# Optimization experiments

Measured on AMD Instinct MI355X. Metric: run time of the kernel, lower is better.

The kernel has to match this reference:

```python
import jax, jax.numpy as jnp
import numpy as np

HEADS = 8
DIM = 512
SCALE = (DIM // HEADS) ** (-0.5)  # 0.125


def setup_inputs() -> dict:
    key = jax.random.key(0)
    k1, k2, k3, k4 = jax.random.split(key, 4)
    B, C, H, W = 4, DIM, 96, 96
    x = jax.random.normal(k1, (B, C, H, W), dtype=jnp.float32)
    # 1x1 conv weights collapsed to matrices [out_ch, in_ch]
    w_qkv = jax.random.normal(k2, (3 * DIM, DIM), dtype=jnp.float32) * (DIM ** -0.5)
    w_out = jax.random.normal(k3, (DIM, DIM), dtype=jnp.float32) * (DIM ** -0.5)
    b_out = jax.random.normal(k4, (DIM,), dtype=jnp.float32) * 0.01
    return {"x": x, "w_qkv": w_qkv, "w_out": w_out, "b_out": b_out}


def reference(x, w_qkv, w_out, b_out):
    # axis='height' branch of the original forward
    b, c, h, w = x.shape
    heads = HEADS
    d = c // heads
    # 1x1 conv == per-pixel GEMM: [B,3C,H,W]
    qkv = jnp.einsum('bchw,oc->bohw', x, w_qkv)
    # 'b (qkv heads d) x y -> qkv b heads x y d'
    qkv = qkv.reshape(b, 3, heads, d, h, w)
    qkv = jnp.transpose(qkv, (1, 0, 2, 4, 5, 3))  # [3, b, heads, h, w, d]
    q, k, v = qkv[0], qkv[1], qkv[2]
    # attention along the width axis, batched over (b, heads, row x)
    dots = jnp.einsum('bhxid,bhxjd->bhxij', q, k) * SCALE
    attn = jax.nn.softmax(dots, axis=-1)
    out = jnp.einsum('bhxij,bhxjd->bhxid', attn, v)  # [b, heads, h, w, d]
    # 'b heads x y d -> b (heads d) x y'
    out = jnp.transpose(out, (0, 1, 4, 2, 3)).reshape(b, heads * d, h, w)
    # to_out 1x1 conv with bias
    out = jnp.einsum('bchw,oc->bohw', out, w_out) + b_out[None, :, None, None]
    return out
```

## Files before the change

kernel.cpp:

```cpp
#include <hip/hip_runtime.h>

typedef unsigned short u16;
typedef unsigned int u32;
typedef __attribute__((ext_vector_type(8))) short short8;
typedef __attribute__((ext_vector_type(4))) float floatx4;

#define HEADS 8
#define DIM 512
#define HH 96
#define WW 96
#define NPIX 9216
#define M_TOT 36864
#define N_QKV 1536
#define SCALE 0.125f

__device__ __forceinline__ float b2f(u16 v){
    union{float f;u32 u;}x; x.u=((u32)v)<<16; return x.f;
}
__device__ __forceinline__ u16 f2b(float f){
    union{float f;u32 u;}x; x.f=f;
    u32 u=x.u + 0x7fffu + ((x.u>>16)&1u);
    return (u16)(u>>16);
}
__device__ __forceinline__ u32 pack2(float a,float b){
    u32 r; asm("v_cvt_pk_bf16_f32 %0, %1, %2" : "=v"(r) : "v"(a), "v"(b));
    return r;
}

__device__ __forceinline__ void gload16(const u16* g, u16* l){
    __builtin_amdgcn_global_load_lds(
        (const __attribute__((address_space(1))) u32*)g,
        (__attribute__((address_space(3))) u32*)l, 16, 0, 0);
}

__global__ void detect_dtype(const u16* __restrict__ wq, int* __restrict__ flag){
    __shared__ int cnt;
    if (threadIdx.x==0) cnt=0;
    __syncthreads();
    u16 u = wq[2*threadIdx.x];
    int e = (u>>7)&0xff;
    if (e>=100 && e<=128) atomicAdd(&cnt,1);
    __syncthreads();
    if (threadIdx.x==0) *flag = (cnt>128)?1:0;
}

__global__ __launch_bounds__(256)
void convert_w(const void* __restrict__ wq, const void* __restrict__ wo,
               const int* __restrict__ flag, u16* __restrict__ wqb, u16* __restrict__ wob){
    const int isb = *flag;
    int i = blockIdx.x*256 + threadIdx.x;
    const int nq = N_QKV*DIM;
    if (i < nq){
        wqb[i] = isb ? ((const u16*)wq)[i] : f2b(((const float*)wq)[i]);
    } else {
        int j = i - nq;
        wob[j] = isb ? ((const u16*)wo)[j] : f2b(((const float*)wo)[j]);
    }
}

__global__ __launch_bounds__(256)
void convert_x(const void* __restrict__ xv, const int* __restrict__ flag,
               u16* __restrict__ xb){
    __shared__ u16 tile[64][65];
    const int isb = *flag;
    const int p0 = blockIdx.x*64, c0 = blockIdx.y*64, b = blockIdx.z;
    const int t = threadIdx.x;
    const int pl = t&63, c4 = t>>6;
    const float* x32 = (const float*)xv;
    const u16*   x16 = (const u16*)xv;
    size_t src = ((size_t)b*DIM + c0 + c4)*NPIX + p0 + pl;
    #pragma unroll
    for (int i=0;i<16;i++){
        int cl = c4 + i*4;
        size_t s = src + (size_t)i*4*NPIX;
        tile[cl][pl] = isb ? x16[s] : f2b(x32[s]);
    }
    __syncthreads();
    const int cu = t&31, r8 = t>>5;
    u32* xb32 = (u32*)xb;
    #pragma unroll
    for (int i=0;i<8;i++){
        int pr = r8 + i*8;
        u32 v = (u32)tile[2*cu][pr] | ((u32)tile[2*cu+1][pr]<<16);
        xb32[((size_t)b*NPIX + p0 + pr)*(DIM/2) + (c0>>1) + cu] = v;
    }
}

__global__ __launch_bounds__(512, 2)
void gemm_qkv(const u16* __restrict__ A, const u16* __restrict__ B,
              u16* __restrict__ Cqk, u16* __restrict__ vt){
    __shared__ __align__(16) union ShMem {
        u16 tiles[65536];
        float ctQ[8][16][68];
        float ctV[8][16][132];
    } sh;
    u16* lds = sh.tiles;
    const int id = blockIdx.x;
    const int xcd = id & 7, slot = id >> 3;
    const int q6 = slot/6;
    const int by = xcd*18 + q6;
    const int bx = slot - q6*6;
    const int t = threadIdx.x;
    const int w = t>>6, l = t&63, lr = l&15, lq = l>>4;
    const int wm2 = w>>2, wn4 = w&3;
    const int m0 = by*256, n0 = bx*256;
    const u16* gA0 = A + (size_t)(m0 +       w*16 + lr)*DIM + lq*8;
    const u16* gA1 = A + (size_t)(m0 + 128 + w*16 + lr)*DIM + lq*8;
    const u16* gB0 = B + (size_t)(n0 +       w*16 + lr)*DIM + lq*8;
    const u16* gB1 = B + (size_t)(n0 + 128 + w*16 + lr)*DIM + lq*8;

#define STG(gp, opb, h, ko, bb) do { \
        const u16* _g = (gp) + (ko); \
        u16* _l = lds + (bb)*32768 + (opb) + ((h)*8 + w)*1024; \
        gload16(_g,      _l); \
        gload16(_g + 32, _l + 512); \
    } while(0)

    floatx4 acc[8][4] = {};
    STG(gA0, 0,     0, 0, 0);
    STG(gA1, 0,     1, 0, 0);
    STG(gB0, 16384, 0, 0, 0);
    STG(gB1, 16384, 1, 0, 0);

    #pragma unroll 1
    for (int ktile=0; ktile<8; ++ktile){
        const int cur = ktile&1, nxt = cur^1;
        const int ko = (ktile+1)*64;
        if (ktile < 7){
            STG(gA0, 0, 0, ko, nxt);
            asm volatile("s_waitcnt vmcnt(2)" ::: "memory");
        } else {
            asm volatile("s_waitcnt vmcnt(0)" ::: "memory");
        }
        __builtin_amdgcn_s_barrier();
        asm volatile("" ::: "memory");
        const u16* bA = lds + cur*32768 +         wm2*8192 + l*8;
        const u16* bB = lds + cur*32768 + 16384 + wn4*4096 + l*8;
        short8 af[4][2], blo[2][2], bhi[2][2];
        #pragma unroll
        for (int mi=0;mi<4;mi++){
            af[mi][0] = *(const short8*)(bA + mi*1024);
            af[mi][1] = *(const short8*)(bA + mi*1024 + 512);
        }
        #pragma unroll
        for (int ni=0;ni<2;ni++){
            blo[ni][0] = *(const short8*)(bB + ni*1024);
            blo[ni][1] = *(const short8*)(bB + ni*1024 + 512);
        }
        if (ktile < 7) STG(gA1, 0, 1, ko, nxt);
        asm volatile("" ::: "memory");
        __builtin_amdgcn_s_barrier();
        __builtin_amdgcn_sched_barrier(0);
        __builtin_amdgcn_s_setprio(1);
        #pragma unroll
        for (int mi=0;mi<4;mi++)
            #pragma unroll
            for (int ni=0;ni<2;ni++){
                acc[mi][ni] = __builtin_amdgcn_mfma_f32_16x16x32_bf16(af[mi][0], blo[ni][0], acc[mi][ni], 0,0,0);
                acc[mi][ni] = __builtin_amdgcn_mfma_f32_16x16x32_bf16(af[mi][1], blo[ni][1], acc[mi][ni], 0,0,0);
            }
        __builtin_amdgcn_s_setprio(0);
        __builtin_amdgcn_sched_barrier(0);
        __builtin_amdgcn_s_barrier();
        #pragma unroll
        for (int ni=0;ni<2;ni++){
            bhi[ni][0] = *(const short8*)(bB + (2+ni)*1024);
            bhi[ni][1] = *(const short8*)(bB + (2+ni)*1024 + 512);
        }
        if (ktile < 7) STG(gB0, 16384, 0, ko, nxt);
        asm volatile("" ::: "memory");
        __builtin_amdgcn_s_barrier();
        __builtin_amdgcn_sched_barrier(0);
        __builtin_amdgcn_s_setprio(1);
        #pragma unroll
        for (int mi=0;mi<4;mi++)
            #pragma unroll
            for (int ni=0;ni<2;ni++){
                acc[mi][2+ni] = __builtin_amdgcn_mfma_f32_16x16x32_bf16(af[mi][0], bhi[ni][0], acc[mi][2+ni], 0,0,0);
                acc[mi][2+ni] = __builtin_amdgcn_mfma_f32_16x16x32_bf16(af[mi][1], bhi[ni][1], acc[mi][2+ni], 0,0,0);
            }
        __builtin_amdgcn_s_setprio(0);
        __builtin_amdgcn_sched_barrier(0);
        __builtin_amdgcn_s_barrier();
        #pragma unroll
        for (int mi=0;mi<4;mi++){
            af[mi][0] = *(const short8*)(bA + (4+mi)*1024);
            af[mi][1] = *(const short8*)(bA + (4+mi)*1024 + 512);
        }
        if (ktile < 7) STG(gB1, 16384, 1, ko, nxt);
        asm volatile("" ::: "memory");
        __builtin_amdgcn_s_barrier();
        __builtin_amdgcn_sched_barrier(0);
        __builtin_amdgcn_s_setprio(1);
        #pragma unroll
        for (int mi=0;mi<4;mi++)
            #pragma unroll
            for (int ni=0;ni<2;ni++){
                acc[4+mi][2+ni] = __builtin_amdgcn_mfma_f32_16x16x32_bf16(af[mi][0], bhi[ni][0], acc[4+mi][2+ni], 0,0,0);
                acc[4+mi][2+ni] = __builtin_amdgcn_mfma_f32_16x16x32_bf16(af[mi][1], bhi[ni][1], acc[4+mi][2+ni], 0,0,0);
            }
        __builtin_amdgcn_s_setprio(0);
        __builtin_amdgcn_sched_barrier(0);
        __builtin_amdgcn_s_barrier();
        __builtin_amdgcn_s_setprio(1);
        #pragma unroll
        for (int mi=0;mi<4;mi++)
            #pragma unroll
            for (int ni=0;ni<2;ni++){
                acc[4+mi][ni] = __builtin_amdgcn_mfma_f32_16x16x32_bf16(af[mi][0], blo[ni][0], acc[4+mi][ni], 0,0,0);
                acc[4+mi][ni] = __builtin_amdgcn_mfma_f32_16x16x32_bf16(af[mi][1], blo[ni][1], acc[4+mi][ni], 0,0,0);
            }
        __builtin_amdgcn_s_setprio(0);
        __builtin_amdgcn_sched_barrier(0);
        asm volatile("" ::: "memory");
        __builtin_amdgcn_s_barrier();
        asm volatile("" ::: "memory");
    }
#undef STG
    if (bx < 4){
        float (*ct)[68] = sh.ctQ[w];
        const int row = l>>2, cg = l&3;
        u16* dstbase = Cqk + (size_t)(m0 + wm2*128)*1024 + n0 + wn4*64 + cg*16;
        #pragma unroll
        for (int mi=0;mi<8;mi++){
            #pragma unroll
            for (int ni=0;ni<4;ni++)
                #pragma unroll
                for (int r=0;r<4;r++)
                    ct[lq*4+r][ni*16+lr] = acc[mi][ni][r];
            const float* cp = &ct[row][cg*16];
            float4 v0 = *(const float4*)(cp);
            float4 v1 = *(const float4*)(cp+4);
            float4 v2 = *(const float4*)(cp+8);
            float4 v3 = *(const float4*)(cp+12);
            uint4 s0, s1;
            s0.x=pack2(v0.x,v0.y); s0.y=pack2(v0.z,v0.w);
            s0.z=pack2(v1.x,v1.y); s0.w=pack2(v1.z,v1.w);
            s1.x=pack2(v2.x,v2.y); s1.y=pack2(v2.z,v2.w);
            s1.z=pack2(v3.x,v3.y); s1.w=pack2(v3.z,v3.w);
            u16* dst = dstbase + (size_t)(mi*16 + row)*1024;
            *((uint4*)dst)     = s0;
            *((uint4*)(dst+8)) = s1;
        }
    } else {
        float (*ct)[132] = sh.ctV[w];
        const int bat  = m0 / NPIX;
        const int pixb = m0 - bat*NPIX + wm2*128;
        const int nl = l>>2, seg = l&3;
        for (int ni=0; ni<4; ni++){
            #pragma unroll
            for (int mi=0;mi<8;mi++)
                #pragma unroll
                for (int r=0;r<4;r++)
                    ct[lr][mi*16 + lq*4 + r] = acc[mi][ni][r];
            int ch  = n0 + wn4*64 + ni*16 + nl - 1024;
            int bh2 = bat*8 + (ch>>6);
            int dd  = ch & 63;
            const float* cp = &ct[nl][seg*32];
            float4 v0 = *(const float4*)(cp);
            float4 v1 = *(const float4*)(cp+4);
            float4 v2 = *(const float4*)(cp+8);
            float4 v3 = *(const float4*)(cp+12);
            float4 v4 = *(const float4*)(cp+16);
            float4 v5 = *(const float4*)(cp+20);
            float4 v6 = *(const float4*)(cp+24);
            float4 v7 = *(const float4*)(cp+28);
            uint4 s0, s1, s2, s3;
            s0.x=pack2(v0.x,v0.y); s0.y=pack2(v0.z,v0.w);
            s0.z=pack2(v1.x,v1.y); s0.w=pack2(v1.z,v1.w);
            s1.x=pack2(v2.x,v2.y); s1.y=pack2(v2.z,v2.w);
            s1.z=pack2(v3.x,v3.y); s1.w=pack2(v3.z,v3.w);
            s2.x=pack2(v4.x,v4.y); s2.y=pack2(v4.z,v4.w);
            s2.z=pack2(v5.x,v5.y); s2.w=pack2(v5.z,v5.w);
            s3.x=pack2(v6.x,v6.y); s3.y=pack2(v6.z,v6.w);
            s3.z=pack2(v7.x,v7.y); s3.w=pack2(v7.z,v7.w);
            u16* dst = vt + (size_t)(bh2*64+dd)*NPIX + pixb + seg*32;
            *((uint4*)dst)      = s0;
            *((uint4*)(dst+8))  = s1;
            *((uint4*)(dst+16)) = s2;
            *((uint4*)(dst+24)) = s3;
        }
    }
}

__global__ __launch_bounds__(256)
void attn_kernel(const u16* __restrict__ qk, const u16* __restrict__ vt,
                 u16* __restrict__ attno){
    __shared__ __align__(16) u16 Qf[6144];
    __shared__ __align__(16) u16 Pb[9984];
    __shared__ float Ss[96][97];
    __shared__ float smax[96][2], ssum[96][2], rinv[96];
    const int t = threadIdx.x;
    const int w = t>>6, l = t&63, lr = l&15, lq = l>>4;
    const int wm = w&1, wn = w>>1;
    const int blk = blockIdx.x;
    const int row  = blk % HH;
    const int bh   = blk / HH;
    const int head = bh & 7;
    const int bat  = bh >> 3;
    const size_t pixrow = (size_t)bat*NPIX + row*WW;
    const u16* qbase = qk + pixrow*1024 + head*64;
    #pragma unroll
    for (int i=0;i<6;i++){
        int c  = w*6 + i;
        int c2 = (c<12) ? c : (c-12);
        int mt = c2>>1, ks = c2&1;
        const u16* g = qbase + (size_t)(mt*16+lr)*1024 + ks*32 + lq*8 + ((c<12)?0:512);
        u16* dst = ((c<12)?Qf:Pb) + c2*512 + l*8;
        gload16(g, dst);
    }
    __syncthreads();
    {
        floatx4 acc[3][3] = {};
        #pragma unroll
        for (int ks=0;ks<2;ks++){
            short8 af[3], bf[3];
            #pragma unroll
            for (int i=0;i<3;i++) af[i] = *(const short8*)&Qf[((wm*3+i)*2+ks)*512 + l*8];
            #pragma unroll
            for (int j=0;j<3;j++) bf[j] = *(const short8*)&Pb[((wn*3+j)*2+ks)*512 + l*8];
            #pragma unroll
            for (int i=0;i<3;i++)
                #pragma unroll
                for (int j=0;j<3;j++)
                    acc[i][j] = __builtin_amdgcn_mfma_f32_16x16x32_bf16(af[i], bf[j], acc[i][j], 0,0,0);
        }
        #pragma unroll
        for (int i=0;i<3;i++)
            #pragma unroll
            for (int j=0;j<3;j++)
                #pragma unroll
                for (int r=0;r<4;r++)
                    Ss[(wm*3+i)*16 + lq*4 + r][(wn*3+j)*16 + lr] = acc[i][j][r]*SCALE;
    }
    __syncthreads();
    #pragma unroll
    for (int i=0;i<3;i++){
        const u16* g = vt + (size_t)(bh*64 + w*16 + lr)*NPIX + row*WW + i*32 + lq*8;
        gload16(g, Qf + (w*3+i)*512 + l*8);
    }
    const int srow = t>>1, shalf = t&1, sbase = shalf*48;
    if (t < 192){
        float m = -1e30f;
        #pragma unroll 8
        for (int j=0;j<48;j++) m = fmaxf(m, Ss[srow][sbase+j]);
        smax[srow][shalf] = m;
    }
    __syncthreads();
    if (t < 192){
        float m2 = fmaxf(smax[srow][0], smax[srow][1]);
        float s = 0.f;
        u32* prow = (u32*)&Pb[srow*104 + sbase];
        #pragma unroll 8
        for (int j=0;j<48;j+=2){
            float e0 = __expf(Ss[srow][sbase+j]   - m2);
            float e1 = __expf(Ss[srow][sbase+j+1] - m2);
            prow[j>>1] = pack2(e0, e1);
            s += e0 + e1;
        }
        ssum[srow][shalf] = s;
    }
    __syncthreads();
    if (t < 192 && shalf==0) rinv[srow] = 1.f/(ssum[srow][0]+ssum[srow][1]);
    floatx4 o[3][2] = {};
    #pragma unroll
    for (int ks2=0;ks2<3;ks2++){
        short8 bf2[2];
        #pragma unroll
        for (int bb=0;bb<2;bb++)
            bf2[bb] = *(const short8*)&Qf[((wn*2+bb)*3+ks2)*512 + l*8];
        #pragma unroll
        for (int aa=0;aa<3;aa++){
            short8 af = *(const short8*)&Pb[((wm*3+aa)*16+lr)*104 + ks2*32 + lq*8];
            #pragma unroll
            for (int bb=0;bb<2;bb++)
                o[aa][bb] = __builtin_amdgcn_mfma_f32_16x16x32_bf16(af, bf2[bb], o[aa][bb], 0,0,0);
        }
    }
    __syncthreads();
    #pragma unroll
    for (int aa=0;aa<3;aa++){
        #pragma unroll
        for (int r=0;r<4;r++){
            int m = (wm*3+aa)*16 + lq*4 + r;
            float rv = rinv[m];
            int d0 = wn*32 + lr;
            Pb[m*72 + d0]      = f2b(o[aa][0][r]*rv);
            Pb[m*72 + d0 + 16] = f2b(o[aa][1][r]*rv);
        }
    }
    __syncthreads();
    #pragma unroll
    for (int i=0;i<3;i++){
        int idx = i*256 + t;
        int rr = idx>>3, seg = idx&7;
        uint4 vv = *(const uint4*)&Pb[rr*72 + seg*8];
        *(uint4*)(attno + (pixrow+rr)*512 + head*64 + seg*8) = vv;
    }
}

__global__ __launch_bounds__(512, 2)
void gemm_out(const u16* __restrict__ A, const u16* __restrict__ B,
              const void* __restrict__ bias, const int* __restrict__ flag,
              void* __restrict__ outv){
    __shared__ __align__(16) union ShMem {
        u16 tiles[65536];
        float ctV[8][16][132];
    } sh;
    u16* lds = sh.tiles;
    const int id = blockIdx.x;
    const int xcd = id & 7, slot = id >> 3;
    const int by = xcd*18 + (slot>>1);
    const int bx = slot & 1;
    const int t = threadIdx.x;
    const int w = t>>6, l = t&63, lr = l&15, lq = l>>4;
    const int wm2 = w>>2, wn4 = w&3;
    const int m0 = by*256, n0 = bx*256;
    const u16* gA0 = A + (size_t)(m0 +       w*16 + lr)*DIM + lq*8;
    const u16* gA1 = A + (size_t)(m0 + 128 + w*16 + lr)*DIM + lq*8;
    const u16* gB0 = B + (size_t)(n0 +       w*16 + lr)*DIM + lq*8;
    const u16* gB1 = B + (size_t)(n0 + 128 + w*16 + lr)*DIM + lq*8;

#define STG(gp, opb, h, ko, bb) do { \
        const u16* _g = (gp) + (ko); \
        u16* _l = lds + (bb)*32768 + (opb) + ((h)*8 + w)*1024; \
        gload16(_g,      _l); \
        gload16(_g + 32, _l + 512); \
    } while(0)

    floatx4 acc[8][4] = {};
    STG(gA0, 0,     0, 0, 0);
    STG(gA1, 0,     1, 0, 0);
    STG(gB0, 16384, 0, 0, 0);
    STG(gB1, 16384, 1, 0, 0);

    #pragma unroll 1
    for (int ktile=0; ktile<8; ++ktile){
        const int cur = ktile&1, nxt = cur^1;
        const int ko = (ktile+1)*64;
        if (ktile < 7){
            STG(gA0, 0, 0, ko, nxt);
            asm volatile("s_waitcnt vmcnt(2)" ::: "memory");
        } else {
            asm volatile("s_waitcnt vmcnt(0)" ::: "memory");
        }
        __builtin_amdgcn_s_barrier();
        asm volatile("" ::: "memory");
        const u16* bA = lds + cur*32768 +         wm2*8192 + l*8;
        const u16* bB = lds + cur*32768 + 16384 + wn4*4096 + l*8;
        short8 af[4][2], blo[2][2], bhi[2][2];
        #pragma unroll
        for (int mi=0;mi<4;mi++){
            af[mi][0] = *(const short8*)(bA + mi*1024);
            af[mi][1] = *(const short8*)(bA + mi*1024 + 512);
        }
        #pragma unroll
        for (int ni=0;ni<2;ni++){
            blo[ni][0] = *(const short8*)(bB + ni*1024);
            blo[ni][1] = *(const short8*)(bB + ni*1024 + 512);
        }
        if (ktile < 7) STG(gA1, 0, 1, ko, nxt);
        asm volatile("" ::: "memory");
        __builtin_amdgcn_s_barrier();
        __builtin_amdgcn_sched_barrier(0);
        __builtin_amdgcn_s_setprio(1);
        #pragma unroll
        for (int mi=0;mi<4;mi++)
            #pragma unroll
            for (int ni=0;ni<2;ni++){
                acc[mi][ni] = __builtin_amdgcn_mfma_f32_16x16x32_bf16(af[mi][0], blo[ni][0], acc[mi][ni], 0,0,0);
                acc[mi][ni] = __builtin_amdgcn_mfma_f32_16x16x32_bf16(af[mi][1], blo[ni][1], acc[mi][ni], 0,0,0);
            }
        __builtin_amdgcn_s_setprio(0);
        __builtin_amdgcn_sched_barrier(0);
        __builtin_amdgcn_s_barrier();
        #pragma unroll
        for (int ni=0;ni<2;ni++){
            bhi[ni][0] = *(const short8*)(bB + (2+ni)*1024);
            bhi[ni][1] = *(const short8*)(bB + (2+ni)*1024 + 512);
        }
        if (ktile < 7) STG(gB0, 16384, 0, ko, nxt);
        asm volatile("" ::: "memory");
        __builtin_amdgcn_s_barrier();
        __builtin_amdgcn_sched_barrier(0);
        __builtin_amdgcn_s_setprio(1);
        #pragma unroll
        for (int mi=0;mi<4;mi++)
            #pragma unroll
            for (int ni=0;ni<2;ni++){
                acc[mi][2+ni] = __builtin_amdgcn_mfma_f32_16x16x32_bf16(af[mi][0], bhi[ni][0], acc[mi][2+ni], 0,0,0);
                acc[mi][2+ni] = __builtin_amdgcn_mfma_f32_16x16x32_bf16(af[mi][1], bhi[ni][1], acc[mi][2+ni], 0,0,0);
            }
        __builtin_amdgcn_s_setprio(0);
        __builtin_amdgcn_sched_barrier(0);
        __builtin_amdgcn_s_barrier();
        #pragma unroll
        for (int mi=0;mi<4;mi++){
            af[mi][0] = *(const short8*)(bA + (4+mi)*1024);
            af[mi][1] = *(const short8*)(bA + (4+mi)*1024 + 512);
        }
        if (ktile < 7) STG(gB1, 16384, 1, ko, nxt);
        asm volatile("" ::: "memory");
        __builtin_amdgcn_s_barrier();
        __builtin_amdgcn_sched_barrier(0);
        __builtin_amdgcn_s_setprio(1);
        #pragma unroll
        for (int mi=0;mi<4;mi++)
            #pragma unroll
            for (int ni=0;ni<2;ni++){
                acc[4+mi][2+ni] = __builtin_amdgcn_mfma_f32_16x16x32_bf16(af[mi][0], bhi[ni][0], acc[4+mi][2+ni], 0,0,0);
                acc[4+mi][2+ni] = __builtin_amdgcn_mfma_f32_16x16x32_bf16(af[mi][1], bhi[ni][1], acc[4+mi][2+ni], 0,0,0);
            }
        __builtin_amdgcn_s_setprio(0);
        __builtin_amdgcn_sched_barrier(0);
        __builtin_amdgcn_s_barrier();
        __builtin_amdgcn_s_setprio(1);
        #pragma unroll
        for (int mi=0;mi<4;mi++)
            #pragma unroll
            for (int ni=0;ni<2;ni++){
                acc[4+mi][ni] = __builtin_amdgcn_mfma_f32_16x16x32_bf16(af[mi][0], blo[ni][0], acc[4+mi][ni], 0,0,0);
                acc[4+mi][ni] = __builtin_amdgcn_mfma_f32_16x16x32_bf16(af[mi][1], blo[ni][1], acc[4+mi][ni], 0,0,0);
            }
        __builtin_amdgcn_s_setprio(0);
        __builtin_amdgcn_sched_barrier(0);
        asm volatile("" ::: "memory");
        __builtin_amdgcn_s_barrier();
        asm volatile("" ::: "memory");
    }
#undef STG
    const int isb = *flag;
    const int bat  = m0 / NPIX;
    const int pix0 = m0 - bat*NPIX + wm2*128;
    float (*ct)[132] = sh.ctV[w];
    const u16*   b16 = (const u16*)bias;
    const float* b32 = (const float*)bias;
    const int nl = l>>3, seg8 = l&7;
    for (int ni=0; ni<4; ni++){
        #pragma unroll
        for (int mi=0;mi<8;mi++)
            #pragma unroll
            for (int r=0;r<4;r++)
                ct[lr][mi*16 + lq*4 + r] = acc[mi][ni][r];
        #pragma unroll
        for (int p=0;p<2;p++){
            int nrow = nl + p*8;
            int ng = n0 + wn4*64 + ni*16 + nrow;
            float bv = isb ? b2f(b16[ng]) : b32[ng];
            const float* cp = &ct[nrow][seg8*16];
            float4 v0 = *(const float4*)(cp);
            float4 v1 = *(const float4*)(cp+4);
            float4 v2 = *(const float4*)(cp+8);
            float4 v3 = *(const float4*)(cp+12);
            v0.x+=bv; v0.y+=bv; v0.z+=bv; v0.w+=bv;
            v1.x+=bv; v1.y+=bv; v1.z+=bv; v1.w+=bv;
            v2.x+=bv; v2.y+=bv; v2.z+=bv; v2.w+=bv;
            v3.x+=bv; v3.y+=bv; v3.z+=bv; v3.w+=bv;
            size_t off = ((size_t)(bat*DIM + ng))*NPIX + pix0 + seg8*16;
            if (isb){
                uint4 s0, s1;
                s0.x=pack2(v0.x,v0.y); s0.y=pack2(v0.z,v0.w);
                s0.z=pack2(v1.x,v1.y); s0.w=pack2(v1.z,v1.w);
                s1.x=pack2(v2.x,v2.y); s1.y=pack2(v2.z,v2.w);
                s1.z=pack2(v3.x,v3.y); s1.w=pack2(v3.z,v3.w);
                *(uint4*)((u16*)outv + off)     = s0;
                *(uint4*)((u16*)outv + off + 8) = s1;
            } else {
                float* of = (float*)outv + off;
                *(float4*)(of)    = v0;
                *(float4*)(of+4)  = v1;
                *(float4*)(of+8)  = v2;
                *(float4*)(of+12) = v3;
            }
        }
    }
}

extern "C" void kernel_launch(void* const* d_in, const int* in_sizes, int n_in,
                              void* d_out, int out_size, void* d_ws, size_t ws_size,
                              hipStream_t stream){
    const void* x    = d_in[0];
    const void* wqkv = d_in[1];
    const void* wout = d_in[2];
    const void* bout = d_in[3];
    char* wsb = (char*)d_ws;
    int* flag    = (int*)wsb;
    u16* xb      = (u16*)(wsb + 256);
    u16* attn_ws = xb;
    u16* wqb     = xb + (size_t)M_TOT*DIM;
    u16* wob     = wqb + (size_t)N_QKV*DIM;
    u16* qk_ws   = wob + (size_t)DIM*DIM;
    u16* vt_ws   = qk_ws + (size_t)M_TOT*1024;
    detect_dtype<<<1, 256, 0, stream>>>((const u16*)wqkv, flag);
    convert_w<<<4096, 256, 0, stream>>>(wqkv, wout, flag, wqb, wob);
    convert_x<<<dim3(144, 8, 4), 256, 0, stream>>>(x, flag, xb);
    gemm_qkv<<<864, 512, 0, stream>>>(xb, wqb, qk_ws, vt_ws);
    attn_kernel<<<3072, 256, 0, stream>>>(qk_ws, vt_ws, attn_ws);
    gemm_out<<<288, 512, 0, stream>>>(attn_ws, wob, bout, flag, d_out);
}
```

Before: 348.6 us.

## Write QKV outputs in attention-fragment order and shrink output GEMM tiles

Result: faster. 340.3 us (-2.4%).

```diff
diff --git a/kernel.cpp b/kernel.cpp
--- a/kernel.cpp
+++ b/kernel.cpp
@@ -88,7 +88,7 @@
 
 __global__ __launch_bounds__(512, 2)
 void gemm_qkv(const u16* __restrict__ A, const u16* __restrict__ B,
-              u16* __restrict__ Cqk, u16* __restrict__ vt){
+              u16* __restrict__ qkt, u16* __restrict__ vtt){
     __shared__ __align__(16) union ShMem {
         u16 tiles[65536];
         float ctQ[8][16][68];
@@ -217,10 +217,15 @@
         asm volatile("" ::: "memory");
     }
 #undef STG
+    const int bat   = m0 / NPIX;
+    const int p0img = (m0 - bat*NPIX) + wm2*128;
     if (bx < 4){
         float (*ct)[68] = sh.ctQ[w];
-        const int row = l>>2, cg = l&3;
-        u16* dstbase = Cqk + (size_t)(m0 + wm2*128)*1024 + n0 + wn4*64 + cg*16;
+        const int nbase = n0 + wn4*64;
+        const int isK   = (nbase >= 512);
+        const int head  = (nbase - (isK ? 512 : 0)) >> 6;
+        const int kqoff = isK ? 6144 : 0;
+        const size_t blk0 = (size_t)(bat*8 + head)*96;
         #pragma unroll
         for (int mi=0;mi<8;mi++){
             #pragma unroll
@@ -228,63 +233,48 @@
                 #pragma unroll
                 for (int r=0;r<4;r++)
                     ct[lq*4+r][ni*16+lr] = acc[mi][ni][r];
-            const float* cp = &ct[row][cg*16];
-            float4 v0 = *(const float4*)(cp);
-            float4 v1 = *(const float4*)(cp+4);
-            float4 v2 = *(const float4*)(cp+8);
-            float4 v3 = *(const float4*)(cp+12);
-            uint4 s0, s1;
-            s0.x=pack2(v0.x,v0.y); s0.y=pack2(v0.z,v0.w);
-            s0.z=pack2(v1.x,v1.y); s0.w=pack2(v1.z,v1.w);
-            s1.x=pack2(v2.x,v2.y); s1.y=pack2(v2.z,v2.w);
-            s1.z=pack2(v3.x,v3.y); s1.w=pack2(v3.z,v3.w);
-            u16* dst = dstbase + (size_t)(mi*16 + row)*1024;
-            *((uint4*)dst)     = s0;
-            *((uint4*)(dst+8)) = s1;
+            int pv  = (p0img + mi*16) >> 4;
+            int row = pv/6, mt = pv - row*6;
+            u16* dst = qkt + (blk0 + row)*12288 + kqoff + mt*1024 + l*8;
+            #pragma unroll
+            for (int ks=0;ks<2;ks++){
+                const float* cp = &ct[l&15][ks*32 + (l>>4)*8];
+                float4 v0 = *(const float4*)(cp);
+                float4 v1 = *(const float4*)(cp+4);
+                uint4 s;
+                s.x=pack2(v0.x,v0.y); s.y=pack2(v0.z,v0.w);
+                s.z=pack2(v1.x,v1.y); s.w=pack2(v1.z,v1.w);
+                *((uint4*)(dst + ks*512)) = s;
+            }
         }
     } else {
         float (*ct)[132] = sh.ctV[w];
-        const int bat  = m0 / NPIX;
-        const int pixb = m0 - bat*NPIX + wm2*128;
-        const int nl = l>>2, seg = l&3;
+        const int head = ((n0 - 1024) + wn4*64) >> 6;
+        const size_t blk0 = (size_t)(bat*8 + head)*96;
         for (int ni=0; ni<4; ni++){
             #pragma unroll
             for (int mi=0;mi<8;mi++)
                 #pragma unroll
                 for (int r=0;r<4;r++)
                     ct[lr][mi*16 + lq*4 + r] = acc[mi][ni][r];
-            int ch  = n0 + wn4*64 + ni*16 + nl - 1024;
-            int bh2 = bat*8 + (ch>>6);
-            int dd  = ch & 63;
-            const float* cp = &ct[nl][seg*32];
-            float4 v0 = *(const float4*)(cp);
-            float4 v1 = *(const float4*)(cp+4);
-            float4 v2 = *(const float4*)(cp+8);
-            float4 v3 = *(const float4*)(cp+12);
-            float4 v4 = *(const float4*)(cp+16);
-            float4 v5 = *(const float4*)(cp+20);
-            float4 v6 = *(const float4*)(cp+24);
-            float4 v7 = *(const float4*)(cp+28);
-            uint4 s0, s1, s2, s3;
-            s0.x=pack2(v0.x,v0.y); s0.y=pack2(v0.z,v0.w);
-            s0.z=pack2(v1.x,v1.y); s0.w=pack2(v1.z,v1.w);
-            s1.x=pack2(v2.x,v2.y); s1.y=pack2(v2.z,v2.w);
-            s1.z=pack2(v3.x,v3.y); s1.w=pack2(v3.z,v3.w);
-            s2.x=pack2(v4.x,v4.y); s2.y=pack2(v4.z,v4.w);
-            s2.z=pack2(v5.x,v5.y); s2.w=pack2(v5.z,v5.w);
-            s3.x=pack2(v6.x,v6.y); s3.y=pack2(v6.z,v6.w);
-            s3.z=pack2(v7.x,v7.y); s3.w=pack2(v7.z,v7.w);
-            u16* dst = vt + (size_t)(bh2*64+dd)*NPIX + pixb + seg*32;
-            *((uint4*)dst)      = s0;
-            *((uint4*)(dst+8))  = s1;
-            *((uint4*)(dst+16)) = s2;
-            *((uint4*)(dst+24)) = s3;
+            #pragma unroll
+            for (int cc=0;cc<4;cc++){
+                int p32 = (p0img + cc*32) >> 5;
+                int row = p32/3, jt = p32 - row*3;
+                const float* cp = &ct[l&15][cc*32 + (l>>4)*8];
+                float4 v0 = *(const float4*)(cp);
+                float4 v1 = *(const float4*)(cp+4);
+                uint4 s;
+                s.x=pack2(v0.x,v0.y); s.y=pack2(v0.z,v0.w);
+                s.z=pack2(v1.x,v1.y); s.w=pack2(v1.z,v1.w);
+                *((uint4*)(vtt + (blk0 + row)*6144 + (ni*3 + jt)*512 + l*8)) = s;
+            }
         }
     }
 }
 
 __global__ __launch_bounds__(256)
-void attn_kernel(const u16* __restrict__ qk, const u16* __restrict__ vt,
+void attn_kernel(const u16* __restrict__ qkt, const u16* __restrict__ vtt,
                  u16* __restrict__ attno){
     __shared__ __align__(16) u16 Qf[6144];
     __shared__ __align__(16) u16 Pb[9984];
@@ -299,15 +289,12 @@
     const int head = bh & 7;
     const int bat  = bh >> 3;
     const size_t pixrow = (size_t)bat*NPIX + row*WW;
-    const u16* qbase = qk + pixrow*1024 + head*64;
+    const u16* qkbase = qkt + (size_t)blk*12288;
     #pragma unroll
     for (int i=0;i<6;i++){
         int c  = w*6 + i;
-        int c2 = (c<12) ? c : (c-12);
-        int mt = c2>>1, ks = c2&1;
-        const u16* g = qbase + (size_t)(mt*16+lr)*1024 + ks*32 + lq*8 + ((c<12)?0:512);
-        u16* dst = ((c<12)?Qf:Pb) + c2*512 + l*8;
-        gload16(g, dst);
+        u16* dst = ((c<12) ? Qf + c*512 : Pb + (c-12)*512) + l*8;
+        gload16(qkbase + c*512 + l*8, dst);
     }
     __syncthreads();
     {
@@ -334,10 +321,13 @@
                     Ss[(wm*3+i)*16 + lq*4 + r][(wn*3+j)*16 + lr] = acc[i][j][r]*SCALE;
     }
     __syncthreads();
-    #pragma unroll
-    for (int i=0;i<3;i++){
-        const u16* g = vt + (size_t)(bh*64 + w*16 + lr)*NPIX + row*WW + i*32 + lq*8;
-        gload16(g, Qf + (w*3+i)*512 + l*8);
+    {
+        const u16* vbase = vtt + (size_t)blk*6144;
+        #pragma unroll
+        for (int i=0;i<3;i++){
+            int c = w*3 + i;
+            gload16(vbase + c*512 + l*8, Qf + c*512 + l*8);
+        }
     }
     const int srow = t>>1, shalf = t&1, sbase = shalf*48;
     if (t < 192){
@@ -404,51 +394,52 @@
               const void* __restrict__ bias, const int* __restrict__ flag,
               void* __restrict__ outv){
     __shared__ __align__(16) union ShMem {
-        u16 tiles[65536];
-        float ctV[8][16][132];
+        u16 tiles[49152];
+        float ct[8][16][68];
     } sh;
     u16* lds = sh.tiles;
     const int id = blockIdx.x;
     const int xcd = id & 7, slot = id >> 3;
-    const int by = xcd*18 + (slot>>1);
-    const int bx = slot & 1;
+    const int by = xcd*18 + (slot>>2);
+    const int bx = slot & 3;
     const int t = threadIdx.x;
     const int w = t>>6, l = t&63, lr = l&15, lq = l>>4;
-    const int wm2 = w>>2, wn4 = w&3;
-    const int m0 = by*256, n0 = bx*256;
-    const u16* gA0 = A + (size_t)(m0 +       w*16 + lr)*DIM + lq*8;
-    const u16* gA1 = A + (size_t)(m0 + 128 + w*16 + lr)*DIM + lq*8;
-    const u16* gB0 = B + (size_t)(n0 +       w*16 + lr)*DIM + lq*8;
-    const u16* gB1 = B + (size_t)(n0 + 128 + w*16 + lr)*DIM + lq*8;
-
-#define STG(gp, opb, h, ko, bb) do { \
-        const u16* _g = (gp) + (ko); \
-        u16* _l = lds + (bb)*32768 + (opb) + ((h)*8 + w)*1024; \
+    const int wm4 = w>>1, wn2 = w&1;
+    const int m0 = by*256, n0 = bx*128;
+    const u16* gA = A + (size_t)(m0 + w*16 + lr)*DIM + lq*8;
+    const u16* gB = B + (size_t)(n0 + w*16 + lr)*DIM + lq*8;
+
+#define STG_A(h, ko, bb) do { \
+        const u16* _g = gA + (size_t)(h)*65536 + (ko); \
+        u16* _l = lds + (bb)*24576 + ((h)*8 + w)*1024; \
         gload16(_g,      _l); \
         gload16(_g + 32, _l + 512); \
     } while(0)
-
-    floatx4 acc[8][4] = {};
-    STG(gA0, 0,     0, 0, 0);
-    STG(gA1, 0,     1, 0, 0);
-    STG(gB0, 16384, 0, 0, 0);
-    STG(gB1, 16384, 1, 0, 0);
+#define STG_B(ko, bb) do { \
+        const u16* _g = gB + (ko); \
+        u16* _l = lds + (bb)*24576 + 16384 + w*1024; \
+        gload16(_g,      _l); \
+        gload16(_g + 32, _l + 512); \
+    } while(0)
+
+    floatx4 acc[4][4] = {};
+    STG_A(0,0,0); STG_A(1,0,0); STG_B(0,0);
 
     #pragma unroll 1
-    for (int ktile=0; ktile<8; ++ktile){
-        const int cur = ktile&1, nxt = cur^1;
-        const int ko = (ktile+1)*64;
-        if (ktile < 7){
-            STG(gA0, 0, 0, ko, nxt);
+    for (int kt=0; kt<8; ++kt){
+        const int cur = kt&1, nxt = cur^1;
+        const int ko = (kt+1)*64;
+        if (kt < 7){
+            STG_A(0, ko, nxt);
             asm volatile("s_waitcnt vmcnt(2)" ::: "memory");
         } else {
             asm volatile("s_waitcnt vmcnt(0)" ::: "memory");
         }
         __builtin_amdgcn_s_barrier();
         asm volatile("" ::: "memory");
-        const u16* bA = lds + cur*32768 +         wm2*8192 + l*8;
-        const u16* bB = lds + cur*32768 + 16384 + wn4*4096 + l*8;
-        short8 af[4][2], blo[2][2], bhi[2][2];
+        const u16* bA = lds + cur*24576 +         wm4*4096 + l*8;
+        const u16* bB = lds + cur*24576 + 16384 + wn2*4096 + l*8;
+        short8 af[4][2], bf[2][2];
         #pragma unroll
         for (int mi=0;mi<4;mi++){
             af[mi][0] = *(const short8*)(bA + mi*1024);
@@ -456,10 +447,10 @@
         }
         #pragma unroll
         for (int ni=0;ni<2;ni++){
-            blo[ni][0] = *(const short8*)(bB + ni*1024);
-            blo[ni][1] = *(const short8*)(bB + ni*1024 + 512);
-        }
-        if (ktile < 7) STG(gA1, 0, 1, ko, nxt);
+            bf[ni][0] = *(const short8*)(bB + ni*1024);
+            bf[ni][1] = *(const short8*)(bB + ni*1024 + 512);
+        }
+        if (kt < 7) STG_A(1, ko, nxt);
         asm volatile("" ::: "memory");
         __builtin_amdgcn_s_barrier();
         __builtin_amdgcn_sched_barrier(0);
@@ -468,18 +459,18 @@
         for (int mi=0;mi<4;mi++)
             #pragma unroll
             for (int ni=0;ni<2;ni++){
-                acc[mi][ni] = __builtin_amdgcn_mfma_f32_16x16x32_bf16(af[mi][0], blo[ni][0], acc[mi][ni], 0,0,0);
-                acc[mi][ni] = __builtin_amdgcn_mfma_f32_16x16x32_bf16(af[mi][1], blo[ni][1], acc[mi][ni], 0,0,0);
+                acc[mi][ni] = __builtin_amdgcn_mfma_f32_16x16x32_bf16(af[mi][0], bf[ni][0], acc[mi][ni], 0,0,0);
+                acc[mi][ni] = __builtin_amdgcn_mfma_f32_16x16x32_bf16(af[mi][1], bf[ni][1], acc[mi][ni], 0,0,0);
             }
         __builtin_amdgcn_s_setprio(0);
         __builtin_amdgcn_sched_barrier(0);
         __builtin_amdgcn_s_barrier();
         #pragma unroll
         for (int ni=0;ni<2;ni++){
-            bhi[ni][0] = *(const short8*)(bB + (2+ni)*1024);
-            bhi[ni][1] = *(const short8*)(bB + (2+ni)*1024 + 512);
-        }
-        if (ktile < 7) STG(gB0, 16384, 0, ko, nxt);
+            bf[ni][0] = *(const short8*)(bB + (2+ni)*1024);
+            bf[ni][1] = *(const short8*)(bB + (2+ni)*1024 + 512);
+        }
+        if (kt < 7) STG_B(ko, nxt);
         asm volatile("" ::: "memory");
         __builtin_amdgcn_s_barrier();
         __builtin_amdgcn_sched_barrier(0);
@@ -488,90 +479,56 @@
         for (int mi=0;mi<4;mi++)
             #pragma unroll
             for (int ni=0;ni<2;ni++){
-                acc[mi][2+ni] = __builtin_amdgcn_mfma_f32_16x16x32_bf16(af[mi][0], bhi[ni][0], acc[mi][2+ni], 0,0,0);
-                acc[mi][2+ni] = __builtin_amdgcn_mfma_f32_16x16x32_bf16(af[mi][1], bhi[ni][1], acc[mi][2+ni], 0,0,0);
+                acc[mi][2+ni] = __builtin_amdgcn_mfma_f32_16x16x32_bf16(af[mi][0], bf[ni][0], acc[mi][2+ni], 0,0,0);
+                acc[mi][2+ni] = __builtin_amdgcn_mfma_f32_16x16x32_bf16(af[mi][1], bf[ni][1], acc[mi][2+ni], 0,0,0);
             }
         __builtin_amdgcn_s_setprio(0);
         __builtin_amdgcn_sched_barrier(0);
-        __builtin_amdgcn_s_barrier();
-        #pragma unroll
-        for (int mi=0;mi<4;mi++){
-            af[mi][0] = *(const short8*)(bA + (4+mi)*1024);
-            af[mi][1] = *(const short8*)(bA + (4+mi)*1024 + 512);
-        }
-        if (ktile < 7) STG(gB1, 16384, 1, ko, nxt);
-        asm volatile("" ::: "memory");
-        __builtin_amdgcn_s_barrier();
-        __builtin_amdgcn_sched_barrier(0);
-        __builtin_amdgcn_s_setprio(1);
-        #pragma unroll
-        for (int mi=0;mi<4;mi++)
-            #pragma unroll
-            for (int ni=0;ni<2;ni++){
-                acc[4+mi][2+ni] = __builtin_amdgcn_mfma_f32_16x16x32_bf16(af[mi][0], bhi[ni][0], acc[4+mi][2+ni], 0,0,0);
-                acc[4+mi][2+ni] = __builtin_amdgcn_mfma_f32_16x16x32_bf16(af[mi][1], bhi[ni][1], acc[4+mi][2+ni], 0,0,0);
-            }
-        __builtin_amdgcn_s_setprio(0);
-        __builtin_amdgcn_sched_barrier(0);
-        __builtin_amdgcn_s_barrier();
-        __builtin_amdgcn_s_setprio(1);
-        #pragma unroll
-        for (int mi=0;mi<4;mi++)
-            #pragma unroll
-            for (int ni=0;ni<2;ni++){
-                acc[4+mi][ni] = __builtin_amdgcn_mfma_f32_16x16x32_bf16(af[mi][0], blo[ni][0], acc[4+mi][ni], 0,0,0);
-                acc[4+mi][ni] = __builtin_amdgcn_mfma_f32_16x16x32_bf16(af[mi][1], blo[ni][1], acc[4+mi][ni], 0,0,0);
-            }
-        __builtin_amdgcn_s_setprio(0);
-        __builtin_amdgcn_sched_barrier(0);
-        asm volatile("" ::: "memory");
-        __builtin_amdgcn_s_barrier();
-        asm volatile("" ::: "memory");
-    }
-#undef STG
+        asm volatile("" ::: "memory");
+        __builtin_amdgcn_s_barrier();
+        asm volatile("" ::: "memory");
+    }
+#undef STG_A
+#undef STG_B
     const int isb = *flag;
     const int bat  = m0 / NPIX;
-    const int pix0 = m0 - bat*NPIX + wm2*128;
-    float (*ct)[132] = sh.ctV[w];
+    const int pix0 = (m0 - bat*NPIX) + wm4*64;
+    float (*ct)[68] = sh.ct[w];
     const u16*   b16 = (const u16*)bias;
     const float* b32 = (const float*)bias;
-    const int nl = l>>3, seg8 = l&7;
+    const int nl = l>>2, seg = l&3;
     for (int ni=0; ni<4; ni++){
         #pragma unroll
-        for (int mi=0;mi<8;mi++)
+        for (int mi=0;mi<4;mi++)
             #pragma unroll
             for (int r=0;r<4;r++)
                 ct[lr][mi*16 + lq*4 + r] = acc[mi][ni][r];
-        #pragma unroll
-        for (int p=0;p<2;p++){
-            int nrow = nl + p*8;
-            int ng = n0 + wn4*64 + ni*16 + nrow;
-            float bv = isb ? b2f(b16[ng]) : b32[ng];
-            const float* cp = &ct[nrow][seg8*16];
-            float4 v0 = *(const float4*)(cp);
-            float4 v1 = *(const float4*)(cp+4);
-            float4 v2 = *(const float4*)(cp+8);
-            float4 v3 = *(const float4*)(cp+12);
-            v0.x+=bv; v0.y+=bv; v0.z+=bv; v0.w+=bv;
-            v1.x+=bv; v1.y+=bv; v1.z+=bv; v1.w+=bv;
-            v2.x+=bv; v2.y+=bv; v2.z+=bv; v2.w+=bv;
-            v3.x+=bv; v3.y+=bv; v3.z+=bv; v3.w+=bv;
-            size_t off = ((size_t)(bat*DIM + ng))*NPIX + pix0 + seg8*16;
-            if (isb){
-                uint4 s0, s1;
-                s0.x=pack2(v0.x,v0.y); s0.y=pack2(v0.z,v0.w);
-                s0.z=pack2(v1.x,v1.y); s0.w=pack2(v1.z,v1.w);
-                s1.x=pack2(v2.x,v2.y); s1.y=pack2(v2.z,v2.w);
-                s1.z=pack2(v3.x,v3.y); s1.w=pack2(v3.z,v3.w);
-                *(uint4*)((u16*)outv + off)     = s0;
-                *(uint4*)((u16*)outv + off + 8) = s1;
-            } else {
-                float* of = (float*)outv + off;
-                *(float4*)(of)    = v0;
-                *(float4*)(of+4)  = v1;
-                *(float4*)(of+8)  = v2;
-                *(float4*)(of+12) = v3;
-            }
+        int ng = n0 + wn2*64 + ni*16 + nl;
+        float bv = isb ? b2f(b16[ng]) : b32[ng];
+        const float* cp = &ct[nl][seg*16];
+        float4 v0 = *(const float4*)(cp);
+        float4 v1 = *(const float4*)(cp+4);
+        float4 v2 = *(const float4*)(cp+8);
+        float4 v3 = *(const float4*)(cp+12);
+        v0.x+=bv; v0.y+=bv; v0.z+=bv; v0.w+=bv;
+        v1.x+=bv; v1.y+=bv; v1.z+=bv; v1.w+=bv;
+        v2.x+=bv; v2.y+=bv; v2.z+=bv; v2.w+=bv;
+        v3.x+=bv; v3.y+=bv; v3.z+=bv; v3.w+=bv;
+        size_t off = ((size_t)(bat*DIM + ng))*NPIX + pix0 + seg*16;
+        if (isb){
+            uint4 s0, s1;
+            s0.x=pack2(v0.x,v0.y); s0.y=pack2(v0.z,v0.w);
+            s0.z=pack2(v1.x,v1.y); s0.w=pack2(v1.z,v1.w);
+            s1.x=pack2(v2.x,v2.y); s1.y=pack2(v2.z,v2.w);
+            s1.z=pack2(v3.x,v3.y); s1.w=pack2(v3.z,v3.w);
+            *(uint4*)((u16*)outv + off)     = s0;
+            *(uint4*)((u16*)outv + off + 8) = s1;
+        } else {
+            float* of = (float*)outv + off;
+            *(float4*)(of)    = v0;
+            *(float4*)(of+4)  = v1;
+            *(float4*)(of+8)  = v2;
+            *(float4*)(of+12) = v3;
         }
     }
 }
@@ -596,5 +553,5 @@
     convert_x<<<dim3(144, 8, 4), 256, 0, stream>>>(x, flag, xb);
     gemm_qkv<<<864, 512, 0, stream>>>(xb, wqb, qk_ws, vt_ws);
     attn_kernel<<<3072, 256, 0, stream>>>(qk_ws, vt_ws, attn_ws);
-    gemm_out<<<288, 512, 0, stream>>>(attn_ws, wob, bout, flag, d_out);
-}
+    gemm_out<<<576, 512, 0, stream>>>(attn_ws, wob, bout, flag, d_out);
+}
```
